# Kernel tuning notes

Measured on AMD Instinct MI355X. Metric: run time of the kernel, lower is better.

## Reference

```python
import jax, jax.numpy as jnp
import numpy as np

N_EMBD = 512
HEAD_SIZE = 64
END_TOKEN = 32000  # == vocab_size


def setup_inputs() -> dict:
    key = jax.random.key(0)
    k1, k2, k3, k4, k5 = jax.random.split(key, 5)
    B, T = 16, 2048
    x = jax.random.normal(k1, (B, T, N_EMBD), dtype=jnp.float32)
    idx = jax.random.randint(k2, (B, T), 0, END_TOKEN)  # never hits END_TOKEN
    s = 1.0 / np.sqrt(N_EMBD)
    Wk = jax.random.normal(k3, (N_EMBD, HEAD_SIZE), dtype=jnp.float32) * s
    Wq = jax.random.normal(k4, (N_EMBD, HEAD_SIZE), dtype=jnp.float32) * s
    Wv = jax.random.normal(k5, (N_EMBD, HEAD_SIZE), dtype=jnp.float32) * s
    return {"x": x, "Wk": Wk, "Wq": Wq, "Wv": Wv, "idx": idx}


def reference(x, Wk, Wq, Wv, idx):
    B, T, C = x.shape
    k = x @ Wk  # [B,T,H]
    q = x @ Wq
    v = x @ Wv
    # end-token mask: zero out query rows at positions >= first end-token position
    is_end = idx == END_TOKEN                       # [B,T]
    has_end = jnp.any(is_end, axis=1)               # [B]
    first_end = jnp.argmax(is_end, axis=1)          # [B], 0 if none
    pos = jnp.arange(T)
    row_ok = jnp.where(has_end[:, None], pos[None, :] < first_end[:, None], True)  # [B,T]
    causal = jnp.tril(jnp.ones((T, T), dtype=bool))
    mask = causal[None, :, :] & row_ok[:, :, None]  # [B,T,T]
    # NOTE: original scales by C**-0.5 with C = n_embd, not head_size
    wei = jnp.einsum('bqh,bkh->bqk', q, k) * (C ** -0.5)
    wei = jnp.where(mask, wei, -jnp.inf)
    wei = jax.nn.softmax(wei, axis=-1)
    out = jnp.einsum('bqk,bkh->bqh', wei, v)  # [B,T,H]
    return out
```

## Files before the change

### kernel.cpp

```cpp
#include <hip/hip_runtime.h>
#include <hip/hip_bf16.h>


#define B_ 16
#define T_ 2048
#define C_ 512
#define LOG2E 1.4426950408889634f

typedef __attribute__((ext_vector_type(4))) float f32x4;
typedef __attribute__((ext_vector_type(8))) short bf16x8;

__device__ inline unsigned short f2bf(float f) {
    unsigned int u = __builtin_bit_cast(unsigned int, f);
    u += 0x7fff + ((u >> 16) & 1);
    return (unsigned short)(u >> 16);
}

__device__ inline f32x4 mfma16(bf16x8 a, bf16x8 b, f32x4 c) {
    return __builtin_amdgcn_mfma_f32_16x16x32_bf16(a, b, c, 0, 0, 0);
}

__global__ void prep_kernel(const float* __restrict__ Wk, const float* __restrict__ Wq,
                            const float* __restrict__ Wv, unsigned short* __restrict__ Wt,
                            int* __restrict__ fe) {
    if (blockIdx.x == 384) {
        if (threadIdx.x < B_) fe[threadIdx.x] = T_;
        return;
    }
    int id = blockIdx.x * 256 + threadIdx.x;
    int n = id >> 9, k = id & 511;
    int mtx = n >> 6, nl = n & 63;
    const float* W = (mtx == 0) ? Wk : ((mtx == 1) ? Wq : Wv);
    float v = W[k * 64 + nl];
    if (mtx == 1) v *= 0.04419417382415922f;
    Wt[n * 512 + k] = f2bf(v);
}

__global__ void scan_kernel(const int* __restrict__ idx, int* __restrict__ fe) {
    int i = blockIdx.x * 256 + threadIdx.x;
    if (idx[i] == 32000) atomicMin(&fe[i >> 11], i & 2047);
}

__global__ __launch_bounds__(256) void qkv_kernel(
        const float* __restrict__ x, const unsigned short* __restrict__ Wt,
        unsigned short* __restrict__ Qm, unsigned short* __restrict__ Km,
        unsigned short* __restrict__ Vt) {
    __shared__ __align__(16) char smem[32768];
    unsigned short* xs  = (unsigned short*)smem;
    unsigned short* wsh = (unsigned short*)(smem + 8192);
    unsigned short* co  = (unsigned short*)smem;
    unsigned short* vco = (unsigned short*)(smem + 17408);

    int tid = threadIdx.x, wave = tid >> 6, lane = tid & 63;
    int m16 = lane & 15, quad = lane >> 4;
    int row0 = blockIdx.x * 64;

    int xrow[2], xcol[2], wrow[6], wcol[6];
#pragma unroll
    for (int i = 0; i < 2; i++) { int u = tid + i * 256; xrow[i] = u >> 3; xcol[i] = (u & 7) * 8; }
#pragma unroll
    for (int i = 0; i < 6; i++) { int u = tid + i * 256; wrow[i] = u >> 3; wcol[i] = (u & 7) * 8; }

    f32x4 xa[2][2]; bf16x8 wr[6];
#pragma unroll
    for (int i = 0; i < 2; i++) {
        const f32x4* p = (const f32x4*)(x + (long)(row0 + xrow[i]) * C_ + xcol[i]);
        xa[i][0] = p[0]; xa[i][1] = p[1];
    }
#pragma unroll
    for (int i = 0; i < 6; i++) wr[i] = *(const bf16x8*)&Wt[wrow[i] * C_ + wcol[i]];

    f32x4 ka[4], qa[4], va[4];
#pragma unroll
    for (int i = 0; i < 4; i++) {
        ka[i] = (f32x4){0.f, 0.f, 0.f, 0.f};
        qa[i] = (f32x4){0.f, 0.f, 0.f, 0.f};
        va[i] = (f32x4){0.f, 0.f, 0.f, 0.f};
    }

    for (int kb = 0; kb < C_; kb += 64) {
        __syncthreads();
#pragma unroll
        for (int i = 0; i < 2; i++) {
            bf16x8 t;
#pragma unroll
            for (int j = 0; j < 4; j++) t[j] = (short)f2bf(xa[i][0][j]);
#pragma unroll
            for (int j = 0; j < 4; j++) t[4 + j] = (short)f2bf(xa[i][1][j]);
            *(bf16x8*)&xs[xrow[i] * 64 + (xcol[i] ^ ((xrow[i] & 7) * 8))] = t;
        }
#pragma unroll
        for (int i = 0; i < 6; i++)
            *(bf16x8*)&wsh[wrow[i] * 64 + (wcol[i] ^ ((wrow[i] & 7) * 8))] = wr[i];
        int kn = kb + 64;
        if (kn < C_) {
#pragma unroll
            for (int i = 0; i < 2; i++) {
                const f32x4* p = (const f32x4*)(x + (long)(row0 + xrow[i]) * C_ + kn + xcol[i]);
                xa[i][0] = p[0]; xa[i][1] = p[1];
            }
#pragma unroll
            for (int i = 0; i < 6; i++) wr[i] = *(const bf16x8*)&Wt[wrow[i] * C_ + kn + wcol[i]];
        }
        __syncthreads();
#pragma unroll
        for (int ks = 0; ks < 2; ks++) {
            int ko = ks * 32 + quad * 8;
            bf16x8 xf[4];
#pragma unroll
            for (int mt = 0; mt < 4; mt++) {
                int ar = mt * 16 + m16;
                xf[mt] = *(const bf16x8*)&xs[ar * 64 + (ko ^ ((ar & 7) * 8))];
            }
            int kr = wave * 16 + m16, qr = 64 + wave * 16 + m16, vr = 128 + wave * 16 + m16;
            bf16x8 wk = *(const bf16x8*)&wsh[kr * 64 + (ko ^ ((kr & 7) * 8))];
            bf16x8 wq = *(const bf16x8*)&wsh[qr * 64 + (ko ^ ((qr & 7) * 8))];
            bf16x8 wv = *(const bf16x8*)&wsh[vr * 64 + (ko ^ ((vr & 7) * 8))];
#pragma unroll
            for (int mt = 0; mt < 4; mt++) ka[mt] = mfma16(xf[mt], wk, ka[mt]);
#pragma unroll
            for (int mt = 0; mt < 4; mt++) qa[mt] = mfma16(xf[mt], wq, qa[mt]);
#pragma unroll
            for (int mt = 0; mt < 4; mt++) va[mt] = mfma16(wv, xf[mt], va[mt]);
        }
    }
    __syncthreads();

#pragma unroll
    for (int mt = 0; mt < 4; mt++) {
        int trow = mt * 16 + quad * 4;
#pragma unroll
        for (int r = 0; r < 4; r++) {
            co[(trow + r) * 136 + wave * 16 + m16]      = f2bf(ka[mt][r]);
            co[(trow + r) * 136 + 64 + wave * 16 + m16] = f2bf(qa[mt][r]);
            vco[wave * 1152 + (quad * 4 + r) * 72 + mt * 16 + m16] = f2bf(va[mt][r]);
        }
    }
    __syncthreads();
#pragma unroll
    for (int i = 0; i < 4; i++) {
        int u = tid + i * 256; int tok = u >> 4; int fg = u & 15;
        bf16x8 vv = *(const bf16x8*)&co[tok * 136 + fg * 8];
        unsigned short* dst = (fg < 8) ? Km : Qm;
        *(bf16x8*)&dst[(long)(row0 + tok) * 64 + (fg & 7) * 8] = vv;
    }
    int bb = row0 >> 11, tl = row0 & 2047;
#pragma unroll
    for (int i = 0; i < 2; i++) {
        int u = lane + i * 64; int hl = u >> 3; int tg = u & 7;
        bf16x8 vv = *(const bf16x8*)&vco[wave * 1152 + hl * 72 + tg * 8];
        *(bf16x8*)&Vt[((long)bb * 64 + wave * 16 + hl) * T_ + tl + tg * 8] = vv;
    }
}

__global__ __launch_bounds__(512, 4) void attn_kernel(
        const unsigned short* __restrict__ Qm, const unsigned short* __restrict__ Km,
        const unsigned short* __restrict__ Vt, const int* __restrict__ fe,
        float* __restrict__ out) {
    __shared__ __align__(16) unsigned short Klds[2][2][64 * 64];
    __shared__ __align__(16) unsigned short Vlds[2][2][64 * 64];
    __shared__ __align__(16) unsigned short Plds[8][16 * 64];

    int id = blockIdx.x;
    int j = id & 255, hi = id >> 8;
    int qt = hi ? 31 - (j >> 3) : (j >> 3);
    int b = (j & 7) | (hi << 3);

    int tid = threadIdx.x, wave = tid >> 6, lane = tid & 63;
    int g = wave >> 2, wg = wave & 3;
    int m16 = lane & 15, quad = lane >> 4;
    int row0 = qt * 64;
    long bT = (long)b * T_;

    int n = qt + 1;
    int n0 = (n + 1) >> 1;
    int n1 = n - n0;
    int ng = g ? n1 : n0;
    int kbase = g ? n0 : 0;
    int nloop = n0;

    int gtid = wg * 64 + lane;
    int srow[2], sk8[2], ssw[2];
#pragma unroll
    for (int c = 0; c < 2; c++) {
        int cc = gtid + c * 256;
        srow[c] = cc >> 3; sk8[c] = (cc & 7) * 8;
        ssw[c] = sk8[c] ^ ((srow[c] & 7) * 8);
    }

    const unsigned short* qp = Qm + (bT + row0 + wg * 16 + m16) * 64;
    bf16x8 qf0 = *(const bf16x8*)(qp + quad * 8);
    bf16x8 qf1 = *(const bf16x8*)(qp + 32 + quad * 8);

    f32x4 o[5];
#pragma unroll
    for (int h = 0; h < 5; h++) o[h] = (f32x4){0.f, 0.f, 0.f, 0.f};
    float mi[4];
#pragma unroll
    for (int r = 0; r < 4; r++) mi[r] = -INFINITY;
    int qloc = row0 + wg * 16 + quad * 4;

    bf16x8 onesb;
    {
        short ov = (m16 == 0) ? (short)0x3F80 : (short)0;
#pragma unroll
        for (int jj = 0; jj < 8; jj++) onesb[jj] = ov;
    }

    unsigned short (*Kg)[64 * 64] = Klds[g];
    unsigned short (*Vg)[64 * 64] = Vlds[g];

    bf16x8 kp[2], vp[2];
    if (ng > 0) {
        long c0 = (long)kbase * 64;
#pragma unroll
        for (int c = 0; c < 2; c++) {
            kp[c] = *(const bf16x8*)&Km[(bT + c0 + srow[c]) * 64 + sk8[c]];
            vp[c] = *(const bf16x8*)&Vt[((long)b * 64 + srow[c]) * T_ + c0 + sk8[c]];
        }
#pragma unroll
        for (int c = 0; c < 2; c++) {
            *(bf16x8*)&Kg[0][srow[c] * 64 + ssw[c]] = kp[c];
            *(bf16x8*)&Vg[0][srow[c] * 64 + ssw[c]] = vp[c];
        }
    }

    for (int it = 0; it < nloop; ++it) {
        int cur = it & 1;
        bool active = it < ng;
        int kt = kbase + it;
        bool pf = active && (it + 1 < ng);
        if (pf) {
            long cn = (long)(kt + 1) * 64;
#pragma unroll
            for (int c = 0; c < 2; c++) {
                kp[c] = *(const bf16x8*)&Km[(bT + cn + srow[c]) * 64 + sk8[c]];
                vp[c] = *(const bf16x8*)&Vt[((long)b * 64 + srow[c]) * T_ + cn + sk8[c]];
            }
        }
        __syncthreads();
        if (active) {
            const unsigned short* Kb = Kg[cur];
            const unsigned short* Vb = Vg[cur];

            f32x4 s[4];
#pragma unroll
            for (int ns = 0; ns < 4; ns++) {
                int krow = ns * 16 + m16;
                int swz = (krow & 7) * 8;
                bf16x8 kf0 = *(const bf16x8*)&Kb[krow * 64 + ((quad * 8) ^ swz)];
                bf16x8 kf1 = *(const bf16x8*)&Kb[krow * 64 + ((32 + quad * 8) ^ swz)];
                f32x4 z = (f32x4){0.f, 0.f, 0.f, 0.f};
                z = mfma16(qf0, kf0, z);
                z = mfma16(qf1, kf1, z);
                s[ns] = z;
            }

            bool diag = (kt == qt);
#pragma unroll
            for (int r = 0; r < 4; r++) {
                int qpos = qloc + r;
                if (diag) {
#pragma unroll
                    for (int ns = 0; ns < 4; ns++) {
                        int nn = kt * 64 + ns * 16 + m16;
                        if (nn > qpos) s[ns][r] = -INFINITY;
                    }
                }
                float mx = fmaxf(fmaxf(s[0][r], s[1][r]), fmaxf(s[2][r], s[3][r]));
                mx = fmaxf(mx, mi[r]);
#pragma unroll
                for (int off = 1; off < 16; off <<= 1)
                    mx = fmaxf(mx, __shfl_xor(mx, off));
                float alpha = exp2f((mi[r] - mx) * LOG2E);
                mi[r] = mx;
#pragma unroll
                for (int ns = 0; ns < 4; ns++)
                    s[ns][r] = exp2f((s[ns][r] - mx) * LOG2E);
#pragma unroll
                for (int h = 0; h < 5; h++) o[h][r] *= alpha;
            }

            unsigned short* pw = Plds[wave];
#pragma unroll
            for (int ns = 0; ns < 4; ns++)
#pragma unroll
                for (int r = 0; r < 4; r++) {
                    int mrow = quad * 4 + r;
                    int nn = ns * 16 + m16;
                    pw[mrow * 64 + (nn ^ ((mrow & 7) * 8))] = f2bf(s[ns][r]);
                }

            int aswz = (m16 & 7) * 8;
            bf16x8 pa0 = *(const bf16x8*)&pw[m16 * 64 + ((quad * 8) ^ aswz)];
            bf16x8 pa1 = *(const bf16x8*)&pw[m16 * 64 + ((32 + quad * 8) ^ aswz)];
#pragma unroll
            for (int hs = 0; hs < 4; hs++) {
                int vrow = hs * 16 + m16;
                int vswz = (vrow & 7) * 8;
                bf16x8 vb0 = *(const bf16x8*)&Vb[vrow * 64 + ((quad * 8) ^ vswz)];
                bf16x8 vb1 = *(const bf16x8*)&Vb[vrow * 64 + ((32 + quad * 8) ^ vswz)];
                o[hs] = mfma16(pa0, vb0, o[hs]);
                o[hs] = mfma16(pa1, vb1, o[hs]);
            }
            o[4] = mfma16(pa0, onesb, o[4]);
            o[4] = mfma16(pa1, onesb, o[4]);
        }
        if (pf) {
            int nxt = 1 - cur;
#pragma unroll
            for (int c = 0; c < 2; c++) {
                *(bf16x8*)&Kg[nxt][srow[c] * 64 + ssw[c]] = kp[c];
                *(bf16x8*)&Vg[nxt][srow[c] * 64 + ssw[c]] = vp[c];
            }
        }
    }

    __syncthreads();
    float* Po = (float*)&Klds[0][0][0];
    float* Pm = Po + 64 * 68;
    float* Pl = Pm + 64;
    if (g == 1) {
#pragma unroll
        for (int r = 0; r < 4; r++) {
            int row = wg * 16 + quad * 4 + r;
#pragma unroll
            for (int hs = 0; hs < 4; hs++)
                Po[row * 68 + hs * 16 + m16] = o[hs][r];
            if (m16 == 0) { Pm[row] = mi[r]; Pl[row] = o[4][r]; }
        }
    }
    __syncthreads();
    if (g == 0) {
        int feb = fe[b];
#pragma unroll
        for (int r = 0; r < 4; r++) {
            int row = wg * 16 + quad * 4 + r;
            int t = row0 + row;
            float m1v = Pm[row], l1v = Pl[row];
            float mm = fmaxf(mi[r], m1v);
            float a0 = exp2f((mi[r] - mm) * LOG2E);
            float a1 = exp2f((m1v - mm) * LOG2E);
            float l0 = __shfl(o[4][r], lane & 48);
            float inv = 1.0f / (l0 * a0 + l1v * a1);
            bool dead = (t >= feb);
#pragma unroll
            for (int hs = 0; hs < 4; hs++) {
                float val = dead ? __builtin_nanf("")
                                 : (o[hs][r] * a0 + Po[row * 68 + hs * 16 + m16] * a1) * inv;
                out[(bT + t) * 64 + hs * 16 + m16] = val;
            }
        }
    }
}

extern "C" void kernel_launch(void* const* d_in, const int* in_sizes, int n_in,
                              void* d_out, int out_size, void* d_ws, size_t ws_size,
                              hipStream_t stream) {
    const float* x  = (const float*)d_in[0];
    const float* Wk = (const float*)d_in[1];
    const float* Wq = (const float*)d_in[2];
    const float* Wv = (const float*)d_in[3];
    const int* idx  = (const int*)d_in[4];
    float* out = (float*)d_out;

    char* ws = (char*)d_ws;
    int* fe            = (int*)ws;
    unsigned short* Wt = (unsigned short*)(ws + 1024);
    unsigned short* Qm = (unsigned short*)(ws + 262144);
    unsigned short* Km = (unsigned short*)(ws + 262144 + 4194304);
    unsigned short* Vt = (unsigned short*)(ws + 262144 + 8388608);

    prep_kernel<<<385, 256, 0, stream>>>(Wk, Wq, Wv, Wt, fe);
    scan_kernel<<<128, 256, 0, stream>>>(idx, fe);
    qkv_kernel<<<512, 256, 0, stream>>>(x, Wt, Qm, Km, Vt);
    attn_kernel<<<512, 512, 0, stream>>>(Qm, Km, Vt, fe, out);
}
```

Before: 154.7 us.

## Split attention KV range across four wave groups with 1024-thread blocks

Grows the attention block from 2 to 4 wave groups (1024 threads), each handling a quarter of the key tiles, then merges the four partial softmax states through LDS. Shared memory for K/V/P staging doubles. The block-to-query-tile mapping is also reversed so the heavier tiles are scheduled first. The aim is shorter per-block serial loops and better load balance, at the cost of larger LDS use, lower achievable occupancy, and a longer merge step.

```diff
diff --git a/kernel.cpp b/kernel.cpp
--- a/kernel.cpp
+++ b/kernel.cpp
@@ -153,17 +153,17 @@
     }
 }
 
-__global__ __launch_bounds__(512, 4) void attn_kernel(
+__global__ __launch_bounds__(1024, 4) void attn_kernel(
         const unsigned short* __restrict__ Qm, const unsigned short* __restrict__ Km,
         const unsigned short* __restrict__ Vt, const int* __restrict__ fe,
         float* __restrict__ out) {
-    __shared__ __align__(16) unsigned short Klds[2][2][64 * 64];
-    __shared__ __align__(16) unsigned short Vlds[2][2][64 * 64];
-    __shared__ __align__(16) unsigned short Plds[8][16 * 64];
+    __shared__ __align__(16) unsigned short Klds[4][2][64 * 64];
+    __shared__ __align__(16) unsigned short Vlds[4][2][64 * 64];
+    __shared__ __align__(16) unsigned short Plds[16][16 * 64];
 
     int id = blockIdx.x;
     int j = id & 255, hi = id >> 8;
-    int qt = hi ? 31 - (j >> 3) : (j >> 3);
+    int qt = hi ? (j >> 3) : (31 - (j >> 3));
     int b = (j & 7) | (hi << 3);
 
     int tid = threadIdx.x, wave = tid >> 6, lane = tid & 63;
@@ -173,11 +173,10 @@
     long bT = (long)b * T_;
 
     int n = qt + 1;
-    int n0 = (n + 1) >> 1;
-    int n1 = n - n0;
-    int ng = g ? n1 : n0;
-    int kbase = g ? n0 : 0;
-    int nloop = n0;
+    int qd = n >> 2, rem = n & 3;
+    int ng = qd + (g < rem);
+    int kbase = g * qd + min(g, rem);
+    int nloop = qd + (rem ? 1 : 0);
 
     int gtid = wg * 64 + lane;
     int srow[2], sk8[2], ssw[2];
@@ -317,10 +316,12 @@
     }
 
     __syncthreads();
-    float* Po = (float*)&Klds[0][0][0];
-    float* Pm = Po + 64 * 68;
-    float* Pl = Pm + 64;
-    if (g == 1) {
+    float* Pbase = (float*)&Klds[0][0][0];
+    const int PSTR = 64 * 68 + 128;
+    if (g > 0) {
+        float* Po = Pbase + (g - 1) * PSTR;
+        float* Pm = Po + 64 * 68;
+        float* Pl = Pm + 64;
 #pragma unroll
         for (int r = 0; r < 4; r++) {
             int row = wg * 16 + quad * 4 + r;
@@ -337,17 +338,31 @@
         for (int r = 0; r < 4; r++) {
             int row = wg * 16 + quad * 4 + r;
             int t = row0 + row;
-            float m1v = Pm[row], l1v = Pl[row];
-            float mm = fmaxf(mi[r], m1v);
+            float l0 = __shfl(o[4][r], lane & 48);
+            float mg[3], mm = mi[r];
+#pragma unroll
+            for (int p = 0; p < 3; p++) {
+                mg[p] = Pbase[p * PSTR + 64 * 68 + row];
+                mm = fmaxf(mm, mg[p]);
+            }
             float a0 = exp2f((mi[r] - mm) * LOG2E);
-            float a1 = exp2f((m1v - mm) * LOG2E);
-            float l0 = __shfl(o[4][r], lane & 48);
-            float inv = 1.0f / (l0 * a0 + l1v * a1);
+            float lsum = l0 * a0;
+            float acc[4];
+#pragma unroll
+            for (int hs = 0; hs < 4; hs++) acc[hs] = o[hs][r] * a0;
+#pragma unroll
+            for (int p = 0; p < 3; p++) {
+                float ap = exp2f((mg[p] - mm) * LOG2E);
+                lsum += Pbase[p * PSTR + 64 * 68 + 64 + row] * ap;
+#pragma unroll
+                for (int hs = 0; hs < 4; hs++)
+                    acc[hs] += Pbase[p * PSTR + row * 68 + hs * 16 + m16] * ap;
+            }
+            float inv = 1.0f / lsum;
             bool dead = (t >= feb);
 #pragma unroll
             for (int hs = 0; hs < 4; hs++) {
-                float val = dead ? __builtin_nanf("")
-                                 : (o[hs][r] * a0 + Po[row * 68 + hs * 16 + m16] * a1) * inv;
+                float val = dead ? __builtin_nanf("") : acc[hs] * inv;
                 out[(bT + t) * 64 + hs * 16 + m16] = val;
             }
         }
@@ -374,5 +389,5 @@
     prep_kernel<<<385, 256, 0, stream>>>(Wk, Wq, Wv, Wt, fe);
     scan_kernel<<<128, 256, 0, stream>>>(idx, fe);
     qkv_kernel<<<512, 256, 0, stream>>>(x, Wt, Qm, Km, Vt);
-    attn_kernel<<<512, 512, 0, stream>>>(Qm, Km, Vt, fe, out);
-}
+    attn_kernel<<<512, 1024, 0, stream>>>(Qm, Km, Vt, fe, out);
+}
```

New measurement: 181.1 us. 17.1% more time.

## Split causal attention over KV chunks with partial outputs and merge kernel

Applied to the files above, without the earlier changes.

Replaces the single fused attention launch with a split-KV scheme: each (batch, query tile) is divided into chunks of up to 8 key tiles, each processed by a separate 256-thread block that writes unnormalized outputs, row max and row sum to a workspace. A merge kernel then rescales and combines the partials, normalizes, and applies the end-token mask. This is meant to balance the triangular causal workload across more blocks and raise occupancy, at the cost of extra global traffic for partials and an additional launch. The old fused kernel is kept as a fallback when the workspace is too small.

```diff
diff --git a/kernel.cpp b/kernel.cpp
--- a/kernel.cpp
+++ b/kernel.cpp
@@ -6,6 +6,7 @@
 #define T_ 2048
 #define C_ 512
 #define LOG2E 1.4426950408889634f
+#define PARTF 4224
 
 typedef __attribute__((ext_vector_type(4))) float f32x4;
 typedef __attribute__((ext_vector_type(8))) short bf16x8;
@@ -18,6 +19,12 @@
 
 __device__ inline f32x4 mfma16(bf16x8 a, bf16x8 b, f32x4 c) {
     return __builtin_amdgcn_mfma_f32_16x16x32_bf16(a, b, c, 0, 0, 0);
+}
+
+__device__ inline int chunk_prefix(int qt, int logCH) {
+    int CH = 1 << logCH;
+    int g = qt >> logCH, r = qt & (CH - 1);
+    return ((CH * g * (g + 1)) >> 1) + r * (g + 1);
 }
 
 __global__ void prep_kernel(const float* __restrict__ Wk, const float* __restrict__ Wq,
@@ -153,7 +160,233 @@
     }
 }
 
-__global__ __launch_bounds__(512, 4) void attn_kernel(
+__global__ __launch_bounds__(256, 4) void attn_kernel(
+        const unsigned short* __restrict__ Qm, const unsigned short* __restrict__ Km,
+        const unsigned short* __restrict__ Vt, float* __restrict__ part, int logCH) {
+    __shared__ __align__(16) unsigned short Klds[2][64 * 64];
+    __shared__ __align__(16) unsigned short Vlds[2][64 * 64];
+    __shared__ __align__(16) unsigned short Plds[4][16 * 64];
+
+    int maxcl = 5 - logCH;
+    int id = blockIdx.x;
+    int pair = id >> maxcl;
+    int c = id & ((1 << maxcl) - 1);
+    int qt = 31 - (pair >> 4);
+    int b = pair & 15;
+
+    int n = qt + 1;
+    int CH = 1 << logCH;
+    int nc = (n + CH - 1) >> logCH;
+    if (c >= nc) return;
+    int kbase = c << logCH;
+    int ng = min(CH, n - kbase);
+
+    int tid = threadIdx.x, wave = tid >> 6, lane = tid & 63;
+    int m16 = lane & 15, quad = lane >> 4;
+    int row0 = qt * 64;
+    long bT = (long)b * T_;
+
+    int srow[2], sk8[2], ssw[2];
+#pragma unroll
+    for (int cc2 = 0; cc2 < 2; cc2++) {
+        int cc = tid + cc2 * 256;
+        srow[cc2] = cc >> 3; sk8[cc2] = (cc & 7) * 8;
+        ssw[cc2] = sk8[cc2] ^ ((srow[cc2] & 7) * 8);
+    }
+
+    const unsigned short* qp = Qm + (bT + row0 + wave * 16 + m16) * 64;
+    bf16x8 qf0 = *(const bf16x8*)(qp + quad * 8);
+    bf16x8 qf1 = *(const bf16x8*)(qp + 32 + quad * 8);
+
+    f32x4 o[5];
+#pragma unroll
+    for (int h = 0; h < 5; h++) o[h] = (f32x4){0.f, 0.f, 0.f, 0.f};
+    float mi[4];
+#pragma unroll
+    for (int r = 0; r < 4; r++) mi[r] = -INFINITY;
+    int qloc = row0 + wave * 16 + quad * 4;
+
+    bf16x8 onesb;
+    {
+        short ov = (m16 == 0) ? (short)0x3F80 : (short)0;
+#pragma unroll
+        for (int jj = 0; jj < 8; jj++) onesb[jj] = ov;
+    }
+
+    bf16x8 kp[2], vp[2];
+    {
+        long c0 = (long)kbase * 64;
+#pragma unroll
+        for (int cc = 0; cc < 2; cc++) {
+            kp[cc] = *(const bf16x8*)&Km[(bT + c0 + srow[cc]) * 64 + sk8[cc]];
+            vp[cc] = *(const bf16x8*)&Vt[((long)b * 64 + srow[cc]) * T_ + c0 + sk8[cc]];
+        }
+#pragma unroll
+        for (int cc = 0; cc < 2; cc++) {
+            *(bf16x8*)&Klds[0][srow[cc] * 64 + ssw[cc]] = kp[cc];
+            *(bf16x8*)&Vlds[0][srow[cc] * 64 + ssw[cc]] = vp[cc];
+        }
+    }
+
+    for (int it = 0; it < ng; ++it) {
+        int cur = it & 1;
+        int kt = kbase + it;
+        bool pf = (it + 1 < ng);
+        if (pf) {
+            long cn = (long)(kt + 1) * 64;
+#pragma unroll
+            for (int cc = 0; cc < 2; cc++) {
+                kp[cc] = *(const bf16x8*)&Km[(bT + cn + srow[cc]) * 64 + sk8[cc]];
+                vp[cc] = *(const bf16x8*)&Vt[((long)b * 64 + srow[cc]) * T_ + cn + sk8[cc]];
+            }
+        }
+        __syncthreads();
+        const unsigned short* Kb = Klds[cur];
+        const unsigned short* Vb = Vlds[cur];
+
+        f32x4 s[4];
+#pragma unroll
+        for (int ns = 0; ns < 4; ns++) {
+            int krow = ns * 16 + m16;
+            int swz = (krow & 7) * 8;
+            bf16x8 kf0 = *(const bf16x8*)&Kb[krow * 64 + ((quad * 8) ^ swz)];
+            bf16x8 kf1 = *(const bf16x8*)&Kb[krow * 64 + ((32 + quad * 8) ^ swz)];
+            f32x4 z = (f32x4){0.f, 0.f, 0.f, 0.f};
+            z = mfma16(qf0, kf0, z);
+            z = mfma16(qf1, kf1, z);
+            s[ns] = z;
+        }
+
+        bool diag = (kt == qt);
+#pragma unroll
+        for (int r = 0; r < 4; r++) {
+            int qpos = qloc + r;
+            if (diag) {
+#pragma unroll
+                for (int ns = 0; ns < 4; ns++) {
+                    int nn = kt * 64 + ns * 16 + m16;
+                    if (nn > qpos) s[ns][r] = -INFINITY;
+                }
+            }
+            float mx = fmaxf(fmaxf(s[0][r], s[1][r]), fmaxf(s[2][r], s[3][r]));
+            mx = fmaxf(mx, mi[r]);
+#pragma unroll
+            for (int off = 1; off < 16; off <<= 1)
+                mx = fmaxf(mx, __shfl_xor(mx, off));
+            float alpha = exp2f((mi[r] - mx) * LOG2E);
+            mi[r] = mx;
+#pragma unroll
+            for (int ns = 0; ns < 4; ns++)
+                s[ns][r] = exp2f((s[ns][r] - mx) * LOG2E);
+#pragma unroll
+            for (int h = 0; h < 5; h++) o[h][r] *= alpha;
+        }
+
+        unsigned short* pw = Plds[wave];
+#pragma unroll
+        for (int ns = 0; ns < 4; ns++)
+#pragma unroll
+            for (int r = 0; r < 4; r++) {
+                int mrow = quad * 4 + r;
+                int nn = ns * 16 + m16;
+                pw[mrow * 64 + (nn ^ ((mrow & 7) * 8))] = f2bf(s[ns][r]);
+            }
+
+        int aswz = (m16 & 7) * 8;
+        bf16x8 pa0 = *(const bf16x8*)&pw[m16 * 64 + ((quad * 8) ^ aswz)];
+        bf16x8 pa1 = *(const bf16x8*)&pw[m16 * 64 + ((32 + quad * 8) ^ aswz)];
+#pragma unroll
+        for (int hs = 0; hs < 4; hs++) {
+            int vrow = hs * 16 + m16;
+            int vswz = (vrow & 7) * 8;
+            bf16x8 vb0 = *(const bf16x8*)&Vb[vrow * 64 + ((quad * 8) ^ vswz)];
+            bf16x8 vb1 = *(const bf16x8*)&Vb[vrow * 64 + ((32 + quad * 8) ^ vswz)];
+            o[hs] = mfma16(pa0, vb0, o[hs]);
+            o[hs] = mfma16(pa1, vb1, o[hs]);
+        }
+        o[4] = mfma16(pa0, onesb, o[4]);
+        o[4] = mfma16(pa1, onesb, o[4]);
+
+        if (pf) {
+            int nxt = 1 - cur;
+#pragma unroll
+            for (int cc = 0; cc < 2; cc++) {
+                *(bf16x8*)&Klds[nxt][srow[cc] * 64 + ssw[cc]] = kp[cc];
+                *(bf16x8*)&Vlds[nxt][srow[cc] * 64 + ssw[cc]] = vp[cc];
+            }
+        }
+    }
+
+    int slot = (chunk_prefix(qt, logCH) + c) * 16 + b;
+    float* pp = part + (long)slot * PARTF;
+#pragma unroll
+    for (int r = 0; r < 4; r++) {
+        int row = wave * 16 + quad * 4 + r;
+#pragma unroll
+        for (int hs = 0; hs < 4; hs++)
+            pp[row * 64 + hs * 16 + m16] = o[hs][r];
+        if (m16 == 0) {
+            pp[4096 + row] = mi[r];
+            pp[4096 + 64 + row] = o[4][r];
+        }
+    }
+}
+
+__global__ __launch_bounds__(256) void merge_kernel(
+        const float* __restrict__ part, const int* __restrict__ fe,
+        float* __restrict__ out, int logCH) {
+    int pair = blockIdx.x;
+    int qt = 31 - (pair >> 4);
+    int b = pair & 15;
+    int n = qt + 1;
+    int CH = 1 << logCH;
+    int nc = (n + CH - 1) >> logCH;
+    int s0 = chunk_prefix(qt, logCH);
+
+    int tid = threadIdx.x;
+    int row = tid >> 2, cg = (tid & 3) * 16;
+    int t = qt * 64 + row;
+
+    float mm = -INFINITY;
+    float mv0 = 0.f, mv1 = 0.f, mv2 = 0.f, mv3 = 0.f;
+#pragma unroll
+    for (int c = 0; c < 4; c++) {
+        if (c < nc) {
+            float m = part[(long)((s0 + c) * 16 + b) * PARTF + 4096 + row];
+            if (c == 0) mv0 = m; else if (c == 1) mv1 = m; else if (c == 2) mv2 = m; else mv3 = m;
+            mm = fmaxf(mm, m);
+        }
+    }
+
+    float lsum = 0.f;
+    f32x4 acc0 = {0.f, 0.f, 0.f, 0.f}, acc1 = acc0, acc2 = acc0, acc3 = acc0;
+#pragma unroll
+    for (int c = 0; c < 4; c++) {
+        if (c < nc) {
+            float m = (c == 0) ? mv0 : (c == 1) ? mv1 : (c == 2) ? mv2 : mv3;
+            float a = exp2f((m - mm) * LOG2E);
+            const float* pp = part + (long)((s0 + c) * 16 + b) * PARTF;
+            lsum += pp[4096 + 64 + row] * a;
+            const f32x4* po = (const f32x4*)(pp + row * 64 + cg);
+            acc0 += po[0] * a; acc1 += po[1] * a; acc2 += po[2] * a; acc3 += po[3] * a;
+        }
+    }
+    float inv = 1.0f / lsum;
+    bool dead = (t >= fe[b]);
+    float nanv = __builtin_nanf("");
+    f32x4 r0, r1, r2, r3;
+#pragma unroll
+    for (int j = 0; j < 4; j++) {
+        r0[j] = dead ? nanv : acc0[j] * inv;
+        r1[j] = dead ? nanv : acc1[j] * inv;
+        r2[j] = dead ? nanv : acc2[j] * inv;
+        r3[j] = dead ? nanv : acc3[j] * inv;
+    }
+    f32x4* op = (f32x4*)(out + ((long)b * T_ + t) * 64 + cg);
+    op[0] = r0; op[1] = r1; op[2] = r2; op[3] = r3;
+}
+
+__global__ __launch_bounds__(512, 4) void attn_fused(
         const unsigned short* __restrict__ Qm, const unsigned short* __restrict__ Km,
         const unsigned short* __restrict__ Vt, const int* __restrict__ fe,
         float* __restrict__ out) {
@@ -370,9 +603,21 @@
     unsigned short* Qm = (unsigned short*)(ws + 262144);
     unsigned short* Km = (unsigned short*)(ws + 262144 + 4194304);
     unsigned short* Vt = (unsigned short*)(ws + 262144 + 8388608);
+    size_t partoff = 262144 + 3 * 4194304;
+    float* part = (float*)(ws + partoff);
+
+    int logCH = -1;
+    if (ws_size >= partoff + (size_t)1280 * PARTF * 4) logCH = 3;
+    else if (ws_size >= partoff + (size_t)768 * PARTF * 4) logCH = 4;
+    else if (ws_size >= partoff + (size_t)512 * PARTF * 4) logCH = 5;
 
     prep_kernel<<<385, 256, 0, stream>>>(Wk, Wq, Wv, Wt, fe);
     scan_kernel<<<128, 256, 0, stream>>>(idx, fe);
     qkv_kernel<<<512, 256, 0, stream>>>(x, Wt, Qm, Km, Vt);
-    attn_kernel<<<512, 512, 0, stream>>>(Qm, Km, Vt, fe, out);
-}
+    if (logCH >= 0) {
+        attn_kernel<<<512 * (32 >> logCH), 256, 0, stream>>>(Qm, Km, Vt, part, logCH);
+        merge_kernel<<<512, 256, 0, stream>>>(part, fe, out, logCH);
+    } else {
+        attn_fused<<<512, 512, 0, stream>>>(Qm, Km, Vt, fe, out);
+    }
+}
```

Result: slower. 164.0 us (+6.0%).
